# Kernel optimization log

Measured on AMD Instinct MI355X. Metric: run time of the kernel, lower is better.

The kernel has to match this reference:

```python
import jax, jax.numpy as jnp
import numpy as np

N = 131072   # total circuit nodes (tokens)
D = 128      # token_emb
E = 600000   # total ragged subgraph members (sum of len(pos)+len(pis) over gates)
G = 20000    # number of gates / subgraphs (len(g.gate))


def setup_inputs() -> dict:
    key = jax.random.key(0)
    ks = jax.random.split(key, 6)
    tf_hs = jax.random.normal(ks[0], (N, D), jnp.float32)
    tf_hf = jax.random.normal(ks[1], (N, D), jnp.float32)
    w_hs = jax.random.normal(ks[2], (D,), jnp.float32) / np.sqrt(D)
    w_hf = jax.random.normal(ks[3], (D,), jnp.float32) / np.sqrt(D)
    member_idx = jax.random.randint(ks[4], (E,), 0, N, dtype=jnp.int32)
    segment_ids = jnp.sort(jax.random.randint(ks[5], (E,), 0, G, dtype=jnp.int32))
    return {"tf_hs": tf_hs, "tf_hf": tf_hf, "w_hs": w_hs, "w_hf": w_hf,
            "member_idx": member_idx, "segment_ids": segment_ids}


def _attn_segment_pool(tok, member_idx, segment_ids, w):
    # Fused replacement for the per-gate python loop:
    #   hop[idx] = pool(cat([tok[pos_idx], tok[pis_idx]]))
    # tf_Pooling modeled as attention pooling: softmax(x @ w)-weighted sum per segment.
    x = tok[member_idx]                                  # [E, D] ragged gather
    logits = x @ w                                       # [E]
    m = jax.ops.segment_max(logits, segment_ids, num_segments=G)   # [G]
    m = jnp.where(jnp.isfinite(m), m, 0.0)               # guard empty segments
    p = jnp.exp(logits - m[segment_ids])                 # [E] stable softmax numerator
    z = jax.ops.segment_sum(p, segment_ids, num_segments=G)       # [G]
    attn = p / jnp.maximum(z, 1e-9)[segment_ids]         # [E]
    return jax.ops.segment_sum(attn[:, None] * x, segment_ids, num_segments=G)  # [G, D]


def reference(tf_hs, tf_hf, w_hs, w_hf, member_idx, segment_ids):
    hop_hs = _attn_segment_pool(tf_hs, member_idx, segment_ids, w_hs)
    hop_hf = _attn_segment_pool(tf_hf, member_idx, segment_ids, w_hf)
    return hop_hs, hop_hf
```

## Files before the change

kernel.cpp:

```cpp
#include <hip/hip_runtime.h>
#include <cmath>

#define D 128

__device__ __forceinline__ uint pack_bf16_rne(float a, float b) {
    uint ua = __float_as_uint(a);
    uint ub = __float_as_uint(b);
    ua += 0x7fffu + ((ua >> 16) & 1u);
    ub += 0x7fffu + ((ub >> 16) & 1u);
    return (ua >> 16) | (ub & 0xffff0000u);
}

__global__ __launch_bounds__(256)
void logits_conv_kernel(const float* __restrict__ tf_hs,
                        const float* __restrict__ tf_hf,
                        const float* __restrict__ w_hs,
                        const float* __restrict__ w_hf,
                        float* __restrict__ logit_hs,
                        float* __restrict__ logit_hf,
                        uint* __restrict__ bhs,
                        uint* __restrict__ bhf,
                        int N) {
    const int lane   = threadIdx.x & 63;
    const int nwaves = (gridDim.x * blockDim.x) >> 6;
    const int w0     = (blockIdx.x * blockDim.x + threadIdx.x) >> 6;

    const float2 whs = ((const float2*)w_hs)[lane];
    const float2 whf = ((const float2*)w_hf)[lane];
    const float2* ths = (const float2*)tf_hs;
    const float2* thf = (const float2*)tf_hf;

    for (int r = w0; r < N; r += nwaves) {
        const float2 xh = ths[(size_t)r * 64 + lane];
        const float2 xf = thf[(size_t)r * 64 + lane];
        if (bhs) {
            bhs[(size_t)r * 64 + lane] = pack_bf16_rne(xh.x, xh.y);
            bhf[(size_t)r * 64 + lane] = pack_bf16_rne(xf.x, xf.y);
        }
        float ph = xh.x * whs.x + xh.y * whs.y;
        float pf = xf.x * whf.x + xf.y * whf.y;
        #pragma unroll
        for (int o = 32; o; o >>= 1) {
            ph += __shfl_xor(ph, o);
            pf += __shfl_xor(pf, o);
        }
        if (lane == 0) { logit_hs[r] = ph; logit_hf[r] = pf; }
    }
}

__global__ void starts_kernel(const int* __restrict__ seg,
                              int* __restrict__ starts, int E, int G) {
    const int e = blockIdx.x * blockDim.x + threadIdx.x;
    if (e >= E) return;
    const int s = seg[e];
    if (e == 0) {
        for (int g = 0; g <= s; ++g) starts[g] = 0;
    } else {
        const int sp = seg[e - 1];
        for (int g = sp + 1; g <= s; ++g) starts[g] = e;
    }
    if (e == E - 1) {
        for (int g = s + 1; g <= G; ++g) starts[g] = E;
    }
}

__global__ __launch_bounds__(256, 4)
void pool_kernel_bf16(const uint2* __restrict__ bhs,
                      const uint2* __restrict__ bhf,
                      const float* __restrict__ logit_hs,
                      const float* __restrict__ logit_hf,
                      const int* __restrict__ member_idx,
                      const int* __restrict__ starts,
                      float* __restrict__ out, int G) {
    const int wid  = threadIdx.x >> 6;
    const int lane = threadIdx.x & 63;
    const int wgid = blockIdx.x * (blockDim.x >> 6) + wid;
    if (wgid >= 2 * G) return;
    const int pool = wgid >= G;
    const int gate = pool ? (wgid - G) : wgid;

    const uint2* tok    = pool ? bhf : bhs;
    const float* logit  = pool ? logit_hf : logit_hs;

    const int start = starts[gate];
    const int end   = starts[gate + 1];
    const int cnt   = end - start;

    const int half = lane >> 5;
    const int hl   = lane & 31;

    float4 acc = make_float4(0.f, 0.f, 0.f, 0.f);
    float m, iz;

    if (cnt <= 64) {
        const int  e   = start + lane;
        const bool v   = e < end;
        const int  row = v ? member_idx[e] : 0;
        const float l  = v ? logit[row] : -INFINITY;
        m = l;
        #pragma unroll
        for (int o = 32; o; o >>= 1) m = fmaxf(m, __shfl_xor(m, o));
        float p = v ? __expf(l - m) : 0.f;
        float z = p;
        #pragma unroll
        for (int o = 32; o; o >>= 1) z += __shfl_xor(z, o);
        iz = 1.f / fmaxf(z, 1e-9f);

        for (int j0 = 0; j0 < cnt; j0 += 32) {
            int rj[16]; float pj[16]; uint2 x[16];
            #pragma unroll
            for (int k = 0; k < 16; ++k) {
                const int src = j0 + 2 * k + half;
                rj[k] = __shfl(row, src);
                pj[k] = __shfl(p,   src);
            }
            #pragma unroll
            for (int k = 0; k < 16; ++k)
                x[k] = tok[(size_t)rj[k] * 32 + hl];
            #pragma unroll
            for (int k = 0; k < 16; ++k) {
                acc.x = fmaf(pj[k], __uint_as_float(x[k].x << 16),          acc.x);
                acc.y = fmaf(pj[k], __uint_as_float(x[k].x & 0xffff0000u),  acc.y);
                acc.z = fmaf(pj[k], __uint_as_float(x[k].y << 16),          acc.z);
                acc.w = fmaf(pj[k], __uint_as_float(x[k].y & 0xffff0000u),  acc.w);
            }
        }
    } else {
        m = -INFINITY; float z = 0.f;
        for (int e0 = start; e0 < end; e0 += 64) {
            const int  e   = e0 + lane;
            const bool v   = e < end;
            const int  row = v ? member_idx[e] : 0;
            const float l  = v ? logit[row] : -INFINITY;
            float cm = l;
            #pragma unroll
            for (int o = 32; o; o >>= 1) cm = fmaxf(cm, __shfl_xor(cm, o));
            const float nm = fmaxf(m, cm);
            z *= __expf(m - nm);
            m = nm;
            float pz = v ? __expf(l - m) : 0.f;
            #pragma unroll
            for (int o = 32; o; o >>= 1) pz += __shfl_xor(pz, o);
            z += pz;
        }
        iz = 1.f / fmaxf(z, 1e-9f);

        for (int e0 = start; e0 < end; e0 += 64) {
            const int  e   = e0 + lane;
            const bool v   = e < end;
            const int  row = v ? member_idx[e] : 0;
            const float l  = v ? logit[row] : -INFINITY;
            const float p  = v ? __expf(l - m) : 0.f;
            const int  jn  = min(64, end - e0);
            for (int j0 = 0; j0 < jn; j0 += 32) {
                int rj[16]; float pj[16]; uint2 x[16];
                #pragma unroll
                for (int k = 0; k < 16; ++k) {
                    const int src = j0 + 2 * k + half;
                    rj[k] = __shfl(row, src);
                    pj[k] = __shfl(p,   src);
                }
                #pragma unroll
                for (int k = 0; k < 16; ++k)
                    x[k] = tok[(size_t)rj[k] * 32 + hl];
                #pragma unroll
                for (int k = 0; k < 16; ++k) {
                    acc.x = fmaf(pj[k], __uint_as_float(x[k].x << 16),          acc.x);
                    acc.y = fmaf(pj[k], __uint_as_float(x[k].x & 0xffff0000u),  acc.y);
                    acc.z = fmaf(pj[k], __uint_as_float(x[k].y << 16),          acc.z);
                    acc.w = fmaf(pj[k], __uint_as_float(x[k].y & 0xffff0000u),  acc.w);
                }
            }
        }
    }

    acc.x += __shfl_xor(acc.x, 32);
    acc.y += __shfl_xor(acc.y, 32);
    acc.z += __shfl_xor(acc.z, 32);
    acc.w += __shfl_xor(acc.w, 32);
    if (half == 0) {
        float4* orow = (float4*)(out + ((size_t)pool * G + gate) * D);
        orow[hl] = make_float4(acc.x * iz, acc.y * iz, acc.z * iz, acc.w * iz);
    }
}

__global__ __launch_bounds__(256, 4)
void pool_kernel_f32(const float* __restrict__ tf_hs,
                     const float* __restrict__ tf_hf,
                     const float* __restrict__ logit_hs,
                     const float* __restrict__ logit_hf,
                     const int* __restrict__ member_idx,
                     const int* __restrict__ starts,
                     float* __restrict__ out, int G) {
    const int wid  = threadIdx.x >> 6;
    const int lane = threadIdx.x & 63;
    const int wgid = blockIdx.x * (blockDim.x >> 6) + wid;
    if (wgid >= 2 * G) return;
    const int pool = wgid >= G;
    const int gate = pool ? (wgid - G) : wgid;

    const float2* tok   = (const float2*)(pool ? tf_hf : tf_hs);
    const float*  logit = pool ? logit_hf : logit_hs;

    const int start = starts[gate];
    const int end   = starts[gate + 1];

    float m = -INFINITY, z = 0.f;
    for (int e0 = start; e0 < end; e0 += 64) {
        const int  e   = e0 + lane;
        const bool v   = e < end;
        const int  row = v ? member_idx[e] : 0;
        const float l  = v ? logit[row] : -INFINITY;
        float cm = l;
        #pragma unroll
        for (int o = 32; o; o >>= 1) cm = fmaxf(cm, __shfl_xor(cm, o));
        const float nm = fmaxf(m, cm);
        z *= __expf(m - nm);
        m = nm;
        float pz = v ? __expf(l - m) : 0.f;
        #pragma unroll
        for (int o = 32; o; o >>= 1) pz += __shfl_xor(pz, o);
        z += pz;
    }
    const float izs = 1.f / fmaxf(z, 1e-9f);

    float2 acc = make_float2(0.f, 0.f);
    for (int e0 = start; e0 < end; e0 += 64) {
        const int  e   = e0 + lane;
        const bool v   = e < end;
        const int  row = v ? member_idx[e] : 0;
        const float l  = v ? logit[row] : -INFINITY;
        const float p  = v ? __expf(l - m) : 0.f;
        const int jn = min(64, end - e0);
        for (int j0 = 0; j0 < jn; j0 += 16) {
            int rj[16]; float pj[16]; float2 x[16];
            #pragma unroll
            for (int k = 0; k < 16; ++k) {
                rj[k] = __shfl(row, j0 + k);
                pj[k] = __shfl(p,   j0 + k);
            }
            #pragma unroll
            for (int k = 0; k < 16; ++k)
                x[k] = tok[(size_t)rj[k] * 64 + lane];
            #pragma unroll
            for (int k = 0; k < 16; ++k) {
                acc.x = fmaf(pj[k], x[k].x, acc.x);
                acc.y = fmaf(pj[k], x[k].y, acc.y);
            }
        }
    }
    float2* orow = (float2*)(out + ((size_t)pool * G + gate) * D);
    orow[lane] = make_float2(acc.x * izs, acc.y * izs);
}

extern "C" void kernel_launch(void* const* d_in, const int* in_sizes, int n_in,
                              void* d_out, int out_size, void* d_ws, size_t ws_size,
                              hipStream_t stream) {
    const float* tf_hs = (const float*)d_in[0];
    const float* tf_hf = (const float*)d_in[1];
    const float* w_hs  = (const float*)d_in[2];
    const float* w_hf  = (const float*)d_in[3];
    const int* member_idx  = (const int*)d_in[4];
    const int* segment_ids = (const int*)d_in[5];
    float* out = (float*)d_out;

    const int N = in_sizes[0] / D;
    const int E = in_sizes[4];
    const int G = out_size / (2 * D);

    const size_t bf16_words = (size_t)N * 64;
    const size_t need = 2 * bf16_words * 4 + 2 * (size_t)N * 4 + (size_t)(G + 1) * 4;
    const int nwaves = 2 * G;

    if (ws_size >= need) {
        uint*  bhs      = (uint*)d_ws;
        uint*  bhf      = bhs + bf16_words;
        float* logit_hs = (float*)(bhf + bf16_words);
        float* logit_hf = logit_hs + N;
        int*   starts   = (int*)(logit_hf + N);

        logits_conv_kernel<<<2048, 256, 0, stream>>>(tf_hs, tf_hf, w_hs, w_hf,
                                                     logit_hs, logit_hf, bhs, bhf, N);
        starts_kernel<<<(E + 255) / 256, 256, 0, stream>>>(segment_ids, starts, E, G);
        pool_kernel_bf16<<<(nwaves + 3) / 4, 256, 0, stream>>>(
            (const uint2*)bhs, (const uint2*)bhf, logit_hs, logit_hf,
            member_idx, starts, out, G);
    } else {
        float* logit_hs = (float*)d_ws;
        float* logit_hf = logit_hs + N;
        int*   starts   = (int*)(logit_hf + N);

        logits_conv_kernel<<<2048, 256, 0, stream>>>(tf_hs, tf_hf, w_hs, w_hf,
                                                     logit_hs, logit_hf, nullptr, nullptr, N);
        starts_kernel<<<(E + 255) / 256, 256, 0, stream>>>(segment_ids, starts, E, G);
        pool_kernel_f32<<<(nwaves + 3) / 4, 256, 0, stream>>>(
            tf_hs, tf_hf, logit_hs, logit_hf, member_idx, starts, out, G);
    }
}
```

Measured before the change: 90.72 us.

## Fuse logits/bf16 conversion with segment-starts kernel, use thread-per-row mapping

Merges the logits+bf16 conversion kernel and the segment-starts kernel into one launch, with block ranges split between the two jobs. The row work moves from one wave per row with shuffle reductions to one thread per row using float4 loads and uint4 bf16 stores. This removes a kernel launch and the shuffle reductions. It risks uncoalesced strided memory access across lanes, which could hurt bandwidth.

```diff
diff --git a/kernel.cpp b/kernel.cpp
--- a/kernel.cpp
+++ b/kernel.cpp
@@ -11,57 +11,63 @@
     return (ua >> 16) | (ub & 0xffff0000u);
 }
 
+__device__ __forceinline__ float dot4(float4 x, float4 w) {
+    return fmaf(x.x, w.x, fmaf(x.y, w.y, fmaf(x.z, w.z, x.w * w.w)));
+}
+
 __global__ __launch_bounds__(256)
-void logits_conv_kernel(const float* __restrict__ tf_hs,
-                        const float* __restrict__ tf_hf,
-                        const float* __restrict__ w_hs,
-                        const float* __restrict__ w_hf,
-                        float* __restrict__ logit_hs,
-                        float* __restrict__ logit_hf,
-                        uint* __restrict__ bhs,
-                        uint* __restrict__ bhf,
-                        int N) {
-    const int lane   = threadIdx.x & 63;
-    const int nwaves = (gridDim.x * blockDim.x) >> 6;
-    const int w0     = (blockIdx.x * blockDim.x + threadIdx.x) >> 6;
-
-    const float2 whs = ((const float2*)w_hs)[lane];
-    const float2 whf = ((const float2*)w_hf)[lane];
-    const float2* ths = (const float2*)tf_hs;
-    const float2* thf = (const float2*)tf_hf;
-
-    for (int r = w0; r < N; r += nwaves) {
-        const float2 xh = ths[(size_t)r * 64 + lane];
-        const float2 xf = thf[(size_t)r * 64 + lane];
-        if (bhs) {
-            bhs[(size_t)r * 64 + lane] = pack_bf16_rne(xh.x, xh.y);
-            bhf[(size_t)r * 64 + lane] = pack_bf16_rne(xf.x, xf.y);
-        }
-        float ph = xh.x * whs.x + xh.y * whs.y;
-        float pf = xf.x * whf.x + xf.y * whf.y;
-        #pragma unroll
-        for (int o = 32; o; o >>= 1) {
-            ph += __shfl_xor(ph, o);
-            pf += __shfl_xor(pf, o);
-        }
-        if (lane == 0) { logit_hs[r] = ph; logit_hf[r] = pf; }
-    }
-}
-
-__global__ void starts_kernel(const int* __restrict__ seg,
-                              int* __restrict__ starts, int E, int G) {
-    const int e = blockIdx.x * blockDim.x + threadIdx.x;
-    if (e >= E) return;
-    const int s = seg[e];
-    if (e == 0) {
-        for (int g = 0; g <= s; ++g) starts[g] = 0;
-    } else {
-        const int sp = seg[e - 1];
-        for (int g = sp + 1; g <= s; ++g) starts[g] = e;
-    }
-    if (e == E - 1) {
-        for (int g = s + 1; g <= G; ++g) starts[g] = E;
-    }
+void prep_kernel(const float* __restrict__ tf_hs,
+                 const float* __restrict__ tf_hf,
+                 const float* __restrict__ w_hs,
+                 const float* __restrict__ w_hf,
+                 const int*   __restrict__ seg,
+                 float* __restrict__ logit_hs,
+                 float* __restrict__ logit_hf,
+                 uint4* __restrict__ bhs,
+                 uint4* __restrict__ bhf,
+                 int*   __restrict__ starts,
+                 int N, int E, int G, int RB) {
+    if ((int)blockIdx.x >= RB) {
+        const int e = (blockIdx.x - RB) * blockDim.x + threadIdx.x;
+        if (e >= E) return;
+        const int s = seg[e];
+        if (e == 0) {
+            for (int g = 0; g <= s; ++g) starts[g] = 0;
+        } else {
+            const int sp = seg[e - 1];
+            for (int g = sp + 1; g <= s; ++g) starts[g] = e;
+        }
+        if (e == E - 1) {
+            for (int g = s + 1; g <= G; ++g) starts[g] = E;
+        }
+        return;
+    }
+
+    const int r = blockIdx.x * blockDim.x + threadIdx.x;
+    if (r >= N) return;
+
+    const float4* rh = (const float4*)(tf_hs + (size_t)r * D);
+    const float4* rf = (const float4*)(tf_hf + (size_t)r * D);
+    const float4* wh = (const float4*)w_hs;
+    const float4* wf = (const float4*)w_hf;
+
+    float ah = 0.f, af = 0.f;
+    #pragma unroll 4
+    for (int i = 0; i < 16; ++i) {
+        const float4 xh0 = rh[2 * i], xh1 = rh[2 * i + 1];
+        const float4 xf0 = rf[2 * i], xf1 = rf[2 * i + 1];
+        ah += dot4(xh0, wh[2 * i]) + dot4(xh1, wh[2 * i + 1]);
+        af += dot4(xf0, wf[2 * i]) + dot4(xf1, wf[2 * i + 1]);
+        uint4 ph, pf;
+        ph.x = pack_bf16_rne(xh0.x, xh0.y); ph.y = pack_bf16_rne(xh0.z, xh0.w);
+        ph.z = pack_bf16_rne(xh1.x, xh1.y); ph.w = pack_bf16_rne(xh1.z, xh1.w);
+        pf.x = pack_bf16_rne(xf0.x, xf0.y); pf.y = pack_bf16_rne(xf0.z, xf0.w);
+        pf.z = pack_bf16_rne(xf1.x, xf1.y); pf.w = pack_bf16_rne(xf1.z, xf1.w);
+        bhs[(size_t)r * 16 + i] = ph;
+        bhf[(size_t)r * 16 + i] = pf;
+    }
+    logit_hs[r] = ah;
+    logit_hf[r] = af;
 }
 
 __global__ __launch_bounds__(256, 4)
@@ -184,6 +190,41 @@
     }
 }
 
+__global__ __launch_bounds__(256)
+void logits_kernel_f32(const float* __restrict__ tf_hs,
+                       const float* __restrict__ tf_hf,
+                       const float* __restrict__ w_hs,
+                       const float* __restrict__ w_hf,
+                       const int*   __restrict__ seg,
+                       float* __restrict__ logit_hs,
+                       float* __restrict__ logit_hf,
+                       int*   __restrict__ starts,
+                       int N, int E, int G, int RB) {
+    if ((int)blockIdx.x >= RB) {
+        const int e = (blockIdx.x - RB) * blockDim.x + threadIdx.x;
+        if (e >= E) return;
+        const int s = seg[e];
+        if (e == 0) { for (int g = 0; g <= s; ++g) starts[g] = 0; }
+        else { const int sp = seg[e - 1]; for (int g = sp + 1; g <= s; ++g) starts[g] = e; }
+        if (e == E - 1) { for (int g = s + 1; g <= G; ++g) starts[g] = E; }
+        return;
+    }
+    const int r = blockIdx.x * blockDim.x + threadIdx.x;
+    if (r >= N) return;
+    const float4* rh = (const float4*)(tf_hs + (size_t)r * D);
+    const float4* rf = (const float4*)(tf_hf + (size_t)r * D);
+    const float4* wh = (const float4*)w_hs;
+    const float4* wf = (const float4*)w_hf;
+    float ah = 0.f, af = 0.f;
+    #pragma unroll 8
+    for (int i = 0; i < 32; ++i) {
+        ah += dot4(rh[i], wh[i]);
+        af += dot4(rf[i], wf[i]);
+    }
+    logit_hs[r] = ah;
+    logit_hf[r] = af;
+}
+
 __global__ __launch_bounds__(256, 4)
 void pool_kernel_f32(const float* __restrict__ tf_hs,
                      const float* __restrict__ tf_hf,
@@ -268,9 +309,12 @@
     const int E = in_sizes[4];
     const int G = out_size / (2 * D);
 
+    const int RB = (N + 255) / 256;
+    const int SB = (E + 255) / 256;
+    const int nwaves = 2 * G;
+
     const size_t bf16_words = (size_t)N * 64;
     const size_t need = 2 * bf16_words * 4 + 2 * (size_t)N * 4 + (size_t)(G + 1) * 4;
-    const int nwaves = 2 * G;
 
     if (ws_size >= need) {
         uint*  bhs      = (uint*)d_ws;
@@ -279,9 +323,10 @@
         float* logit_hf = logit_hs + N;
         int*   starts   = (int*)(logit_hf + N);
 
-        logits_conv_kernel<<<2048, 256, 0, stream>>>(tf_hs, tf_hf, w_hs, w_hf,
-                                                     logit_hs, logit_hf, bhs, bhf, N);
-        starts_kernel<<<(E + 255) / 256, 256, 0, stream>>>(segment_ids, starts, E, G);
+        prep_kernel<<<RB + SB, 256, 0, stream>>>(
+            tf_hs, tf_hf, w_hs, w_hf, segment_ids,
+            logit_hs, logit_hf, (uint4*)bhs, (uint4*)bhf, starts,
+            N, E, G, RB);
         pool_kernel_bf16<<<(nwaves + 3) / 4, 256, 0, stream>>>(
             (const uint2*)bhs, (const uint2*)bhf, logit_hs, logit_hf,
             member_idx, starts, out, G);
@@ -290,9 +335,9 @@
         float* logit_hf = logit_hs + N;
         int*   starts   = (int*)(logit_hf + N);
 
-        logits_conv_kernel<<<2048, 256, 0, stream>>>(tf_hs, tf_hf, w_hs, w_hf,
-                                                     logit_hs, logit_hf, nullptr, nullptr, N);
-        starts_kernel<<<(E + 255) / 256, 256, 0, stream>>>(segment_ids, starts, E, G);
+        logits_kernel_f32<<<RB + SB, 256, 0, stream>>>(
+            tf_hs, tf_hf, w_hs, w_hf, segment_ids,
+            logit_hs, logit_hf, starts, N, E, G, RB);
         pool_kernel_f32<<<(nwaves + 3) / 4, 256, 0, stream>>>(
             tf_hs, tf_hf, logit_hs, logit_hf, member_idx, starts, out, G);
     }
```

Result: slower. 123.5 us (+36.1%).
